# Kernel tuning notes

Measured on AMD Instinct MI355X. Metric: run time of the kernel, lower is better.

## Reference

```python
import jax, jax.numpy as jnp
import numpy as np

N = 50000      # nodes
E = 600000     # edges
D = 128        # num_features == hidden_dim
H = 1          # heads (only runnable config of this module)
C = 128        # per-head channels
L = 2          # num_layers
G = 64         # graphs in batch
NC = 10        # num_classes


def setup_inputs() -> dict:
    key = jax.random.key(0)
    ks = jax.random.split(key, 12)
    s = 1.0 / np.sqrt(D)
    inp = {
        "x": jax.random.normal(ks[0], (N, D), jnp.float32),
        "edge_index": jax.random.randint(ks[1], (2, E), 0, N),
        "batch": jnp.sort(jax.random.randint(ks[2], (N,), 0, G)),
        # per-layer TransformerConv params (stacked over layers)
        "Wq": jax.random.normal(ks[3], (L, D, H * C), jnp.float32) * s,
        "bq": jax.random.normal(ks[4], (L, H * C), jnp.float32) * 0.01,
        "Wk": jax.random.normal(ks[5], (L, D, H * C), jnp.float32) * s,
        "bk": jax.random.normal(ks[6], (L, H * C), jnp.float32) * 0.01,
        "Wv": jax.random.normal(ks[7], (L, D, H * C), jnp.float32) * s,
        "bv": jax.random.normal(ks[8], (L, H * C), jnp.float32) * 0.01,
        "Ws": jax.random.normal(ks[9], (L, D, H * C), jnp.float32) * s,  # lin_skip (root weight)
        "bs": jax.random.normal(ks[10], (L, H * C), jnp.float32) * 0.01,
        "W_fc": jax.random.normal(ks[11], (H * C, NC), jnp.float32) * (1.0 / np.sqrt(H * C)),
        "b_fc": jnp.zeros((NC,), jnp.float32),
    }
    return inp


def _transformer_conv(x, src, dst, wq, bq, wk, bk, wv, bv, ws, bs):
    n = x.shape[0]
    q = (x @ wq + bq).reshape(n, H, C)
    k = (x @ wk + bk).reshape(n, H, C)
    v = (x @ wv + bv).reshape(n, H, C)
    # edge-wise gather: query from dst (x_i), key/value from src (x_j)
    score = (q[dst] * k[src]).sum(-1) / jnp.sqrt(jnp.float32(C))  # [E, H]
    # segment softmax over incoming edges of each dst node
    m = jax.ops.segment_max(score, dst, num_segments=n)           # [N, H]
    ex = jnp.exp(score - m[dst])
    den = jax.ops.segment_sum(ex, dst, num_segments=n)
    alpha = ex / den[dst]                                         # [E, H]
    agg = jax.ops.segment_sum(alpha[..., None] * v[src], dst, num_segments=n)
    return agg.reshape(n, H * C) + x @ ws + bs                    # concat heads + skip


def reference(x, edge_index, batch, Wq, bq, Wk, bk, Wv, bv, Ws, bs, W_fc, b_fc):
    src, dst = edge_index[0], edge_index[1]
    h = x
    for l in range(L):
        h = jax.nn.relu(_transformer_conv(h, src, dst, Wq[l], bq[l], Wk[l], bk[l],
                                          Wv[l], bv[l], Ws[l], bs[l]))
    # global mean pool per graph
    sums = jax.ops.segment_sum(h, batch, num_segments=G)
    cnts = jax.ops.segment_sum(jnp.ones((h.shape[0],), h.dtype), batch, num_segments=G)
    pooled = sums / jnp.maximum(cnts, 1.0)[:, None]
    logits = pooled @ W_fc + b_fc
    return jax.nn.log_softmax(logits, axis=1)
```

## Files before the change

kernel.cpp:

```cpp
#include <hip/hip_runtime.h>
#include <math.h>

#define NN 50000
#define EE 600000
#define DD 128
#define GG 64
#define NCLS 10
#define PCHUNK 128
#define NTILE (NN / 16)
#define NBUK 196
#define BSTRIDE 4096
#define EPB ((EE + 255) / 256)

typedef __attribute__((ext_vector_type(8))) __bf16 bf16x8;
typedef __attribute__((ext_vector_type(8))) unsigned short u16x8;
typedef __attribute__((ext_vector_type(4))) float f32x4;
typedef __attribute__((ext_vector_type(2))) float f32x2;

__device__ __forceinline__ unsigned short f2bf(float f) {
    unsigned int u = __float_as_uint(f);
    u += 0x7fff + ((u >> 16) & 1);
    return (unsigned short)(u >> 16);
}

__device__ __forceinline__ float bf2f(unsigned short h) {
    return __uint_as_float(((unsigned int)h) << 16);
}

__device__ __forceinline__ float lo16(unsigned int u) { return __uint_as_float(u << 16); }
__device__ __forceinline__ float hi16(unsigned int u) { return __uint_as_float(u & 0xffff0000u); }


__global__ __launch_bounds__(256) void prep_kernel(
    const float* __restrict__ wq, const float* __restrict__ wk,
    const float* __restrict__ wv, const float* __restrict__ ws,
    const float* __restrict__ x, unsigned short* __restrict__ xb,
    unsigned short* __restrict__ wt,
    int* __restrict__ bucketcnt, float* __restrict__ gsum) {
    int tid = blockIdx.x * 256 + threadIdx.x;
    int TOT = gridDim.x * 256;
    if (tid < 256) bucketcnt[tid] = 0;
    for (int i = tid; i < GG * DD + GG; i += TOT) gsum[i] = 0.f;
    for (int i = tid; i < 2 * 4 * 16384; i += TOT) {
        int k = i & 127;
        int n = (i >> 7) & 127;
        int lm = i >> 14;
        int l = lm >> 2, m = lm & 3;
        const float* w = (m == 0) ? wq : (m == 1) ? wk : (m == 2) ? wv : ws;
        wt[i] = f2bf(w[l * 16384 + k * 128 + n]);
    }
    for (int i = tid; i < NN * DD / 8; i += TOT) {
        const float* px = x + (size_t)i * 8;
        float4 f0 = *(const float4*)px;
        float4 f1 = *(const float4*)(px + 4);
        u16x8 o;
        o[0] = f2bf(f0.x); o[1] = f2bf(f0.y); o[2] = f2bf(f0.z); o[3] = f2bf(f0.w);
        o[4] = f2bf(f1.x); o[5] = f2bf(f1.y); o[6] = f2bf(f1.z); o[7] = f2bf(f1.w);
        *(u16x8*)(xb + (size_t)i * 8) = o;
    }
}


__global__ __launch_bounds__(1024) void bucket_kernel(
    const int* __restrict__ src, const int* __restrict__ dst,
    int* __restrict__ bucketcnt, int2* __restrict__ bedge) {
    __shared__ int hist[256];
    __shared__ int base[256];
    int t = threadIdx.x;
    if (t < 256) hist[t] = 0;
    __syncthreads();
    int e0 = blockIdx.x * EPB;
    int eend = min(e0 + EPB, EE);

    int b0 = -1, b1 = -1, b2 = -1;
    int sl0 = 0, sl1 = 0, sl2 = 0;
    int s0 = 0, s1 = 0, s2 = 0, d0 = 0, d1 = 0, d2 = 0;
    int i = e0 + t;
    if (i < eend) { d0 = dst[i]; s0 = src[i]; b0 = d0 >> 8; sl0 = atomicAdd(&hist[b0], 1); }
    i += 1024;
    if (i < eend) { d1 = dst[i]; s1 = src[i]; b1 = d1 >> 8; sl1 = atomicAdd(&hist[b1], 1); }
    i += 1024;
    if (i < eend) { d2 = dst[i]; s2 = src[i]; b2 = d2 >> 8; sl2 = atomicAdd(&hist[b2], 1); }
    __syncthreads();

    if (t < 256) {
        int h = hist[t];
        base[t] = h ? atomicAdd(&bucketcnt[t], h) : 0;
    }
    __syncthreads();

    if (b0 >= 0) bedge[b0 * BSTRIDE + base[b0] + sl0] = make_int2(s0, d0);
    if (b1 >= 0) bedge[b1 * BSTRIDE + base[b1] + sl1] = make_int2(s1, d1);
    if (b2 >= 0) bedge[b2 * BSTRIDE + base[b2] + sl2] = make_int2(s2, d2);
}


__global__ __launch_bounds__(1024) void bsort_kernel(
    const int* __restrict__ bucketcnt, const int2* __restrict__ bedge,
    int* __restrict__ indptr, int* __restrict__ esrc) {
    __shared__ int buf[256];
    __shared__ int cur[256];
    int b = blockIdx.x;
    int t = threadIdx.x;

    if (t < 256) buf[t] = (t < NBUK) ? bucketcnt[t] : 0;
    __syncthreads();
    if (t < 64) {
        int carry = 0;
        #pragma unroll
        for (int c = 0; c < 4; ++c) {
            int v = buf[c * 64 + t];
            int x = v;
            #pragma unroll
            for (int off = 1; off < 64; off <<= 1) {
                int y = __shfl_up(x, off);
                if (t >= off) x += y;
            }
            cur[c * 64 + t] = carry + x - v;
            carry += __shfl(x, 63);
        }
    }
    __syncthreads();
    int count = buf[b];
    int bstart = cur[b];
    int node0 = b << 8;
    int nn = min(256, NN - node0);
    if (b == 0 && t == 0) indptr[NN] = EE;
    __syncthreads();
    if (t < 256) buf[t] = 0;
    __syncthreads();

    const int2* be = bedge + (size_t)b * BSTRIDE;
    for (int i2 = t; i2 < count; i2 += 1024)
        atomicAdd(&buf[be[i2].y - node0], 1);
    __syncthreads();

    if (t < 64) {
        int carry = 0;
        #pragma unroll
        for (int c = 0; c < 4; ++c) {
            int v = buf[c * 64 + t];
            int x = v;
            #pragma unroll
            for (int off = 1; off < 64; off <<= 1) {
                int y = __shfl_up(x, off);
                if (t >= off) x += y;
            }
            cur[c * 64 + t] = carry + x - v;
            carry += __shfl(x, 63);
        }
    }
    __syncthreads();
    if (t < nn) indptr[node0 + t] = bstart + cur[t];
    __syncthreads();

    for (int i2 = t; i2 < count; i2 += 1024) {
        int2 e = be[i2];
        int slot = atomicAdd(&cur[e.y - node0], 1);
        esrc[bstart + slot] = e.x;
    }
}


__global__ __launch_bounds__(256, 4) void gemm_mfma(
    const unsigned short* __restrict__ xin,
    const unsigned short* __restrict__ wt,
    const float* __restrict__ bq, const float* __restrict__ bk,
    const float* __restrict__ bv, const float* __restrict__ bs,
    unsigned short* __restrict__ qb, unsigned short* __restrict__ kvb,
    unsigned short* __restrict__ sb) {
    __shared__ __align__(16) unsigned short stg[4][16][72];

    int wid = threadIdx.x >> 6;
    int gw = blockIdx.x * 4 + wid;
    int lane = threadIdx.x & 63;
    int mat = (gw >> 1) & 3;
    int ch = gw & 1;
    int wseq = gw >> 3;
    int lr = lane & 15, quad = lane >> 4;

    const unsigned short* wm_ = wt + mat * 16384;
    const float* bias = (mat == 0) ? bq : (mat == 1) ? bk : (mat == 2) ? bv : bs;
    unsigned short* outp; int ostride, ooff;
    if (mat == 0)      { outp = qb;  ostride = 128; ooff = 0; }
    else if (mat == 1) { outp = kvb; ostride = 256; ooff = 0; }
    else if (mat == 2) { outp = kvb; ostride = 256; ooff = 128; }
    else               { outp = sb;  ostride = 128; ooff = 0; }

    bf16x8 bfr[4][4];
    #pragma unroll
    for (int ks = 0; ks < 4; ++ks)
        #pragma unroll
        for (int tn = 0; tn < 4; ++tn)
            bfr[ks][tn] = *(const bf16x8*)(wm_ + (ch * 64 + tn * 16 + lr) * 128
                                               + ks * 32 + quad * 8);
    float bcol[4];
    #pragma unroll
    for (int tn = 0; tn < 4; ++tn) bcol[tn] = bias[ch * 64 + tn * 16 + lr];

    int srow = lane >> 3;
    int sc8 = (lane & 7) * 8;

    for (int tile = wseq; tile < NTILE; tile += 256) {
        int row0 = tile * 16;
        bf16x8 af[4];
        #pragma unroll
        for (int ks = 0; ks < 4; ++ks)
            af[ks] = *(const bf16x8*)(xin + (size_t)(row0 + lr) * DD + ks * 32 + quad * 8);

        f32x4 acc[4];
        #pragma unroll
        for (int tn = 0; tn < 4; ++tn) acc[tn] = (f32x4){0.f, 0.f, 0.f, 0.f};
        #pragma unroll
        for (int ks = 0; ks < 4; ++ks)
            #pragma unroll
            for (int tn = 0; tn < 4; ++tn)
                acc[tn] = __builtin_amdgcn_mfma_f32_16x16x32_bf16(
                    af[ks], bfr[ks][tn], acc[tn], 0, 0, 0);

        #pragma unroll
        for (int tn = 0; tn < 4; ++tn)
            #pragma unroll
            for (int r = 0; r < 4; ++r)
                stg[wid][quad * 4 + r][tn * 16 + lr] = f2bf(acc[tn][r] + bcol[tn]);
        #pragma unroll
        for (int i = 0; i < 2; ++i) {
            int row = i * 8 + srow;
            u16x8 o = *(const u16x8*)&stg[wid][row][sc8];
            *(u16x8*)(outp + (size_t)(row0 + row) * ostride + ooff + ch * 64 + sc8) = o;
        }
    }
}


__global__ __launch_bounds__(256) void kv8_kernel(
    const unsigned short* __restrict__ kvb, unsigned char* __restrict__ kv8) {
    int idx = blockIdx.x * 256 + threadIdx.x;
    int node = idx >> 4, j = idx & 15;
    const unsigned short* base = kvb + (size_t)node * 256;
    uint4 kin = *(const uint4*)(base + j * 8);
    uint4 vin = *(const uint4*)(base + 128 + j * 8);
    unsigned int w0 = __builtin_amdgcn_cvt_pk_fp8_f32(lo16(kin.x), hi16(kin.x), 0, false);
    w0 = __builtin_amdgcn_cvt_pk_fp8_f32(lo16(kin.y), hi16(kin.y), w0, true);
    unsigned int w1 = __builtin_amdgcn_cvt_pk_fp8_f32(lo16(kin.z), hi16(kin.z), 0, false);
    w1 = __builtin_amdgcn_cvt_pk_fp8_f32(lo16(kin.w), hi16(kin.w), w1, true);
    unsigned int w2 = __builtin_amdgcn_cvt_pk_fp8_f32(lo16(vin.x), hi16(vin.x), 0, false);
    w2 = __builtin_amdgcn_cvt_pk_fp8_f32(lo16(vin.y), hi16(vin.y), w2, true);
    unsigned int w3 = __builtin_amdgcn_cvt_pk_fp8_f32(lo16(vin.z), hi16(vin.z), 0, false);
    w3 = __builtin_amdgcn_cvt_pk_fp8_f32(lo16(vin.w), hi16(vin.w), w3, true);
    *(uint4*)(kv8 + (size_t)idx * 16) = make_uint4(w0, w1, w2, w3);
}


__global__ __launch_bounds__(256) void attn_kernel(
    const unsigned short* __restrict__ qb, const unsigned char* __restrict__ kv8,
    const unsigned short* __restrict__ sb,
    const int* __restrict__ indptr, const int* __restrict__ esrc,
    unsigned short* __restrict__ hout, int n) {
    int node = (int)((blockIdx.x * blockDim.x + threadIdx.x) >> 6);
    int lane = threadIdx.x & 63;
    if (node >= n) return;
    int g = lane >> 4, j = lane & 15;

    u16x8 q8 = *(const u16x8*)(qb + (size_t)node * DD + j * 8);
    float qf[8];
    #pragma unroll
    for (int c = 0; c < 8; ++c) qf[c] = bf2f(q8[c]);

    int beg = indptr[node], end = indptr[node + 1];

    float m = -3.0e38f, den = 0.f;
    float acc[8];
    #pragma unroll
    for (int c = 0; c < 8; ++c) acc[c] = 0.f;

    int e = beg + g;
    if (e < end) {
        int sidx = esrc[e];
        int en = e + 4;
        int sn = (en < end) ? esrc[en] : 0;
        uint4 kv = *(const uint4*)(kv8 + (size_t)sidx * 256 + j * 16);
        for (;;) {
            bool haven = en < end;
            int en2 = en + 4;
            int sn2 = (en2 < end) ? esrc[en2] : 0;
            uint4 kvn;
            if (haven)
                kvn = *(const uint4*)(kv8 + (size_t)sn * 256 + j * 16);
            f32x2 k01 = __builtin_amdgcn_cvt_pk_f32_fp8(kv.x, false);
            f32x2 k23 = __builtin_amdgcn_cvt_pk_f32_fp8(kv.x, true);
            f32x2 k45 = __builtin_amdgcn_cvt_pk_f32_fp8(kv.y, false);
            f32x2 k67 = __builtin_amdgcn_cvt_pk_f32_fp8(kv.y, true);
            float p_;
            p_ = qf[0] * k01.x;
            p_ = fmaf(qf[1], k01.y, p_);
            p_ = fmaf(qf[2], k23.x, p_);
            p_ = fmaf(qf[3], k23.y, p_);
            p_ = fmaf(qf[4], k45.x, p_);
            p_ = fmaf(qf[5], k45.y, p_);
            p_ = fmaf(qf[6], k67.x, p_);
            p_ = fmaf(qf[7], k67.y, p_);
            p_ += __shfl_xor(p_, 8);
            p_ += __shfl_xor(p_, 4);
            p_ += __shfl_xor(p_, 2);
            p_ += __shfl_xor(p_, 1);
            float score = p_ * 0.088388347648318447f;
            float mn = fmaxf(m, score);
            float scale = __expf(m - mn);
            float pe = __expf(score - mn);
            den = den * scale + pe;
            f32x2 v01 = __builtin_amdgcn_cvt_pk_f32_fp8(kv.z, false);
            f32x2 v23 = __builtin_amdgcn_cvt_pk_f32_fp8(kv.z, true);
            f32x2 v45 = __builtin_amdgcn_cvt_pk_f32_fp8(kv.w, false);
            f32x2 v67 = __builtin_amdgcn_cvt_pk_f32_fp8(kv.w, true);
            acc[0] = fmaf(acc[0], scale, pe * v01.x);
            acc[1] = fmaf(acc[1], scale, pe * v01.y);
            acc[2] = fmaf(acc[2], scale, pe * v23.x);
            acc[3] = fmaf(acc[3], scale, pe * v23.y);
            acc[4] = fmaf(acc[4], scale, pe * v45.x);
            acc[5] = fmaf(acc[5], scale, pe * v45.y);
            acc[6] = fmaf(acc[6], scale, pe * v67.x);
            acc[7] = fmaf(acc[7], scale, pe * v67.y);
            m = mn;
            if (!haven) break;
            en = en2; sn = sn2; kv = kvn;
        }
    }

    float mo = __shfl_xor(m, 16);
    float m2 = fmaxf(m, mo);
    mo = __shfl_xor(m2, 32);
    float mf = fmaxf(m2, mo);
    float sc = __expf(m - mf);
    den *= sc;
    den += __shfl_xor(den, 16);
    den += __shfl_xor(den, 32);
    #pragma unroll
    for (int c = 0; c < 8; ++c) {
        float a = acc[c] * sc;
        a += __shfl_xor(a, 16);
        a += __shfl_xor(a, 32);
        acc[c] = a;
    }
    float inv = den > 0.f ? 1.0f / den : 0.f;
    if (g == 0) {
        u16x8 s8 = *(const u16x8*)(sb + (size_t)node * DD + j * 8);
        u16x8 o8;
        #pragma unroll
        for (int c = 0; c < 8; ++c)
            o8[c] = f2bf(fmaxf(fmaf(acc[c], inv, bf2f(s8[c])), 0.f));
        *(u16x8*)(hout + (size_t)node * DD + j * 8) = o8;
    }
}


__global__ __launch_bounds__(128) void pool_kernel(const unsigned short* __restrict__ h,
                                                   const int* __restrict__ batch,
                                                   float* __restrict__ gsum,
                                                   float* __restrict__ gcnt, int n) {
    __shared__ int bsh[PCHUNK];
    int t = threadIdx.x;
    int node0 = blockIdx.x * PCHUNK;
    int nnodes = min(PCHUNK, n - node0);
    if (t < nnodes) bsh[t] = batch[node0 + t];
    __syncthreads();

    int cur = bsh[0];
    float acc = 0.f;
    int cnt = 0;
    for (int j = 0; j < nnodes; ++j) {
        int g = bsh[j];
        float val = bf2f(h[(size_t)(node0 + j) * DD + t]);
        if (g != cur) {
            atomicAdd(&gsum[cur * DD + t], acc);
            if (t == 0) atomicAdd(&gcnt[cur], (float)cnt);
            acc = 0.f; cnt = 0; cur = g;
        }
        acc += val; ++cnt;
    }
    if (cnt > 0) {
        atomicAdd(&gsum[cur * DD + t], acc);
        if (t == 0) atomicAdd(&gcnt[cur], (float)cnt);
    }
}


__global__ __launch_bounds__(64) void head_kernel(
    const float* __restrict__ gsum, const float* __restrict__ gcnt,
    const float* __restrict__ wfc, const float* __restrict__ bfc,
    float* __restrict__ out) {
    int g = blockIdx.x;
    int lane = threadIdx.x;
    float cnt = fmaxf(gcnt[g], 1.0f);
    float inv = 1.0f / cnt;
    float p0 = gsum[g * DD + lane] * inv;
    float p1 = gsum[g * DD + lane + 64] * inv;
    __shared__ float logits[NCLS];
    for (int c = 0; c < NCLS; ++c) {
        float partial = p0 * wfc[lane * NCLS + c] + p1 * wfc[(lane + 64) * NCLS + c];
        partial += __shfl_xor(partial, 32);
        partial += __shfl_xor(partial, 16);
        partial += __shfl_xor(partial, 8);
        partial += __shfl_xor(partial, 4);
        partial += __shfl_xor(partial, 2);
        partial += __shfl_xor(partial, 1);
        if (lane == 0) logits[c] = partial + bfc[c];
    }
    __syncthreads();
    if (lane == 0) {
        float mx = logits[0];
        for (int c = 1; c < NCLS; ++c) mx = fmaxf(mx, logits[c]);
        float sum = 0.f;
        for (int c = 0; c < NCLS; ++c) sum += expf(logits[c] - mx);
        float lse = mx + logf(sum);
        for (int c = 0; c < NCLS; ++c) out[g * NCLS + c] = logits[c] - lse;
    }
}


extern "C" void kernel_launch(void* const* d_in, const int* in_sizes, int n_in,
                              void* d_out, int out_size, void* d_ws, size_t ws_size,
                              hipStream_t stream) {
    const float* x     = (const float*)d_in[0];
    const int*   ei    = (const int*)d_in[1];
    const int*   batch = (const int*)d_in[2];
    const float* Wq = (const float*)d_in[3];
    const float* bq = (const float*)d_in[4];
    const float* Wk = (const float*)d_in[5];
    const float* bk = (const float*)d_in[6];
    const float* Wv = (const float*)d_in[7];
    const float* bv = (const float*)d_in[8];
    const float* Ws = (const float*)d_in[9];
    const float* bs = (const float*)d_in[10];
    const float* Wfc = (const float*)d_in[11];
    const float* bfc = (const float*)d_in[12];
    float* out = (float*)d_out;

    const size_t ND = (size_t)NN * DD;
    unsigned short* hbuf = (unsigned short*)d_ws;
    unsigned short* qb  = hbuf + ND;
    unsigned short* sb  = qb + ND;
    unsigned short* kvb = sb + ND;
    unsigned short* wt  = kvb + 2 * ND;
    unsigned char*  kv8 = (unsigned char*)(wt + 2 * 4 * 16384);
    int* bucketcnt = (int*)(kv8 + (size_t)NN * 256);
    int* indptr    = bucketcnt + 256;
    int* esrc      = indptr + NN + 1;
    int2* bedge    = (int2*)(esrc + EE);
    float* gsum = (float*)(bedge + NBUK * BSTRIDE);
    float* gcnt = gsum + GG * DD;
    unsigned short* xb = (unsigned short*)(gcnt + GG);

    const int* src = ei;
    const int* dst = ei + EE;

    prep_kernel<<<512, 256, 0, stream>>>(Wq, Wk, Wv, Ws, x, xb, wt, bucketcnt, gsum);
    bucket_kernel<<<256, 1024, 0, stream>>>(src, dst, bucketcnt, bedge);
    bsort_kernel<<<NBUK, 1024, 0, stream>>>(bucketcnt, bedge, indptr, esrc);

    for (int l = 0; l < 2; ++l) {
        size_t bo = (size_t)l * DD;
        const unsigned short* wtl = wt + (size_t)l * 4 * 16384;
        gemm_mfma<<<512, 256, 0, stream>>>(
            (l == 0) ? xb : hbuf, wtl, bq + bo, bk + bo, bv + bo, bs + bo,
            qb, kvb, sb);
        kv8_kernel<<<(NN * 16) / 256, 256, 0, stream>>>(kvb, kv8);
        attn_kernel<<<(NN + 3) / 4, 256, 0, stream>>>(
            qb, kv8, sb, indptr, esrc, hbuf, NN);
    }

    pool_kernel<<<(NN + PCHUNK - 1) / PCHUNK, 128, 0, stream>>>(hbuf, batch, gsum, gcnt, NN);
    head_kernel<<<GG, 64, 0, stream>>>(gsum, gcnt, Wfc, bfc, out);
}
```

Before: 267.9 us.

## Fuse fp8 K/V conversion into the projection GEMM epilogue

Each block's four waves are regrouped so that one block computes either Q and skip or K and V for the same 16-row tile. The K/V results are staged in shared memory and converted straight to fp8 before being stored, which removes the separate kv8 conversion kernel and the bf16 K/V intermediate buffer with its write and read traffic. In exchange, each tile iteration now needs two block-wide barriers, and the workspace layout is rearranged.

```diff
diff --git a/kernel.cpp b/kernel.cpp
--- a/kernel.cpp
+++ b/kernel.cpp
@@ -167,25 +167,21 @@
     const unsigned short* __restrict__ wt,
     const float* __restrict__ bq, const float* __restrict__ bk,
     const float* __restrict__ bv, const float* __restrict__ bs,
-    unsigned short* __restrict__ qb, unsigned short* __restrict__ kvb,
-    unsigned short* __restrict__ sb) {
-    __shared__ __align__(16) unsigned short stg[4][16][72];
+    unsigned short* __restrict__ qb, unsigned short* __restrict__ sb,
+    unsigned char* __restrict__ kv8) {
+    __shared__ __align__(16) unsigned short stg[2][16][136];
 
     int wid = threadIdx.x >> 6;
-    int gw = blockIdx.x * 4 + wid;
     int lane = threadIdx.x & 63;
-    int mat = (gw >> 1) & 3;
-    int ch = gw & 1;
-    int wseq = gw >> 3;
+    int typeB = blockIdx.x & 1;
+    int mi = wid >> 1;
+    int ch = wid & 1;
+    int mat = typeB ? (mi ? 2 : 1) : (mi ? 3 : 0);
+    int wseq = blockIdx.x >> 1;
     int lr = lane & 15, quad = lane >> 4;
 
     const unsigned short* wm_ = wt + mat * 16384;
     const float* bias = (mat == 0) ? bq : (mat == 1) ? bk : (mat == 2) ? bv : bs;
-    unsigned short* outp; int ostride, ooff;
-    if (mat == 0)      { outp = qb;  ostride = 128; ooff = 0; }
-    else if (mat == 1) { outp = kvb; ostride = 256; ooff = 0; }
-    else if (mat == 2) { outp = kvb; ostride = 256; ooff = 128; }
-    else               { outp = sb;  ostride = 128; ooff = 0; }
 
     bf16x8 bfr[4][4];
     #pragma unroll
@@ -198,8 +194,9 @@
     #pragma unroll
     for (int tn = 0; tn < 4; ++tn) bcol[tn] = bias[ch * 64 + tn * 16 + lr];
 
-    int srow = lane >> 3;
-    int sc8 = (lane & 7) * 8;
+    int t = threadIdx.x;
+    int rr = t >> 4;
+    int cj = t & 15;
 
     for (int tile = wseq; tile < NTILE; tile += 256) {
         int row0 = tile * 16;
@@ -222,33 +219,29 @@
         for (int tn = 0; tn < 4; ++tn)
             #pragma unroll
             for (int r = 0; r < 4; ++r)
-                stg[wid][quad * 4 + r][tn * 16 + lr] = f2bf(acc[tn][r] + bcol[tn]);
-        #pragma unroll
-        for (int i = 0; i < 2; ++i) {
-            int row = i * 8 + srow;
-            u16x8 o = *(const u16x8*)&stg[wid][row][sc8];
-            *(u16x8*)(outp + (size_t)(row0 + row) * ostride + ooff + ch * 64 + sc8) = o;
+                stg[mi][quad * 4 + r][ch * 64 + tn * 16 + lr] = f2bf(acc[tn][r] + bcol[tn]);
+        __syncthreads();
+
+        if (!typeB) {
+            uint4 vq = *(const uint4*)&stg[0][rr][cj * 8];
+            *(uint4*)(qb + (size_t)(row0 + rr) * 128 + cj * 8) = vq;
+            uint4 vs = *(const uint4*)&stg[1][rr][cj * 8];
+            *(uint4*)(sb + (size_t)(row0 + rr) * 128 + cj * 8) = vs;
+        } else {
+            uint4 kk = *(const uint4*)&stg[0][rr][cj * 8];
+            uint4 vv = *(const uint4*)&stg[1][rr][cj * 8];
+            unsigned int w0 = __builtin_amdgcn_cvt_pk_fp8_f32(lo16(kk.x), hi16(kk.x), 0, false);
+            w0 = __builtin_amdgcn_cvt_pk_fp8_f32(lo16(kk.y), hi16(kk.y), w0, true);
+            unsigned int w1 = __builtin_amdgcn_cvt_pk_fp8_f32(lo16(kk.z), hi16(kk.z), 0, false);
+            w1 = __builtin_amdgcn_cvt_pk_fp8_f32(lo16(kk.w), hi16(kk.w), w1, true);
+            unsigned int w2 = __builtin_amdgcn_cvt_pk_fp8_f32(lo16(vv.x), hi16(vv.x), 0, false);
+            w2 = __builtin_amdgcn_cvt_pk_fp8_f32(lo16(vv.y), hi16(vv.y), w2, true);
+            unsigned int w3 = __builtin_amdgcn_cvt_pk_fp8_f32(lo16(vv.z), hi16(vv.z), 0, false);
+            w3 = __builtin_amdgcn_cvt_pk_fp8_f32(lo16(vv.w), hi16(vv.w), w3, true);
+            *(uint4*)(kv8 + (size_t)(row0 + rr) * 256 + cj * 16) = make_uint4(w0, w1, w2, w3);
         }
-    }
-}
-
-
-__global__ __launch_bounds__(256) void kv8_kernel(
-    const unsigned short* __restrict__ kvb, unsigned char* __restrict__ kv8) {
-    int idx = blockIdx.x * 256 + threadIdx.x;
-    int node = idx >> 4, j = idx & 15;
-    const unsigned short* base = kvb + (size_t)node * 256;
-    uint4 kin = *(const uint4*)(base + j * 8);
-    uint4 vin = *(const uint4*)(base + 128 + j * 8);
-    unsigned int w0 = __builtin_amdgcn_cvt_pk_fp8_f32(lo16(kin.x), hi16(kin.x), 0, false);
-    w0 = __builtin_amdgcn_cvt_pk_fp8_f32(lo16(kin.y), hi16(kin.y), w0, true);
-    unsigned int w1 = __builtin_amdgcn_cvt_pk_fp8_f32(lo16(kin.z), hi16(kin.z), 0, false);
-    w1 = __builtin_amdgcn_cvt_pk_fp8_f32(lo16(kin.w), hi16(kin.w), w1, true);
-    unsigned int w2 = __builtin_amdgcn_cvt_pk_fp8_f32(lo16(vin.x), hi16(vin.x), 0, false);
-    w2 = __builtin_amdgcn_cvt_pk_fp8_f32(lo16(vin.y), hi16(vin.y), w2, true);
-    unsigned int w3 = __builtin_amdgcn_cvt_pk_fp8_f32(lo16(vin.z), hi16(vin.z), 0, false);
-    w3 = __builtin_amdgcn_cvt_pk_fp8_f32(lo16(vin.w), hi16(vin.w), w3, true);
-    *(uint4*)(kv8 + (size_t)idx * 16) = make_uint4(w0, w1, w2, w3);
+        __syncthreads();
+    }
 }
 
 
@@ -440,16 +433,15 @@
     unsigned short* hbuf = (unsigned short*)d_ws;
     unsigned short* qb  = hbuf + ND;
     unsigned short* sb  = qb + ND;
-    unsigned short* kvb = sb + ND;
-    unsigned short* wt  = kvb + 2 * ND;
+    unsigned short* wt  = sb + ND;
     unsigned char*  kv8 = (unsigned char*)(wt + 2 * 4 * 16384);
-    int* bucketcnt = (int*)(kv8 + (size_t)NN * 256);
+    unsigned short* xb  = (unsigned short*)(kv8 + (size_t)NN * 256);
+    int* bucketcnt = (int*)(xb + ND);
     int* indptr    = bucketcnt + 256;
     int* esrc      = indptr + NN + 1;
     int2* bedge    = (int2*)(esrc + EE);
     float* gsum = (float*)(bedge + NBUK * BSTRIDE);
     float* gcnt = gsum + GG * DD;
-    unsigned short* xb = (unsigned short*)(gcnt + GG);
 
     const int* src = ei;
     const int* dst = ei + EE;
@@ -463,8 +455,7 @@
         const unsigned short* wtl = wt + (size_t)l * 4 * 16384;
         gemm_mfma<<<512, 256, 0, stream>>>(
             (l == 0) ? xb : hbuf, wtl, bq + bo, bk + bo, bv + bo, bs + bo,
-            qb, kvb, sb);
-        kv8_kernel<<<(NN * 16) / 256, 256, 0, stream>>>(kvb, kv8);
+            qb, sb, kv8);
         attn_kernel<<<(NN + 3) / 4, 256, 0, stream>>>(
             qb, kv8, sb, indptr, esrc, hbuf, NN);
     }
```

Result: faster. 258.4 us (-3.5%).
